# Kernel tuning notes

Measured on AMD Instinct MI355X. Metric: run time of the kernel, lower is better.

The kernel has to match this reference:

```python
import jax, jax.numpy as jnp
import numpy as np

B, N, D = 8, 512, 3


def setup_inputs() -> dict:
    key = jax.random.key(0)
    ks = jax.random.split(key, 9)
    s = lambda fan_in: 1.0 / np.sqrt(fan_in)
    return {
        "coords": jax.random.normal(ks[0], (B, N, D), jnp.float32),
        "fw0": jax.random.normal(ks[1], (3, 64), jnp.float32) * s(3),
        "fb0": jnp.zeros((64,), jnp.float32),
        "fw1": jax.random.normal(ks[2], (64, 128), jnp.float32) * s(64),
        "fb1": jnp.zeros((128,), jnp.float32),
        "aw0": jax.random.normal(ks[3], (6, 64), jnp.float32) * s(6),
        "ab0": jnp.zeros((64,), jnp.float32),
        "aw1": jax.random.normal(ks[4], (64, 64), jnp.float32) * s(64),
        "ab1": jnp.zeros((64,), jnp.float32),
        "aw2": jax.random.normal(ks[5], (64, 1), jnp.float32) * s(64),
        "ab2": jnp.zeros((1,), jnp.float32),
        "uw0": jax.random.normal(ks[6], (259, 256), jnp.float32) * s(259),
        "ub0": jnp.zeros((256,), jnp.float32),
        "uw1": jax.random.normal(ks[7], (256, 128), jnp.float32) * s(256),
        "ub1": jnp.zeros((128,), jnp.float32),
    }


def reference(coords, fw0, fb0, fw1, fb1, aw0, ab0, aw1, ab1, aw2, ab2,
              uw0, ub0, uw1, ub1):
    relu = jax.nn.relu
    # node feature MLP: (B, N, 3) -> (B, N, 128)
    h = relu(relu(coords @ fw0 + fb0) @ fw1 + fb1)
    # pairwise concat: (B, N, N, 2D)
    nP = coords.shape[1]
    pi = jnp.broadcast_to(coords[:, :, None, :], (B, nP, nP, D))
    pj = jnp.broadcast_to(coords[:, None, :, :], (B, nP, nP, D))
    pair = jnp.concatenate([pi, pj], axis=-1)
    # adjacency MLP -> scalar per pair; note final layer also has relu
    a = relu(pair @ aw0 + ab0)
    a = relu(a @ aw1 + ab1)
    A = relu(a @ aw2 + ab2)[..., 0]  # (B, N, N)
    # aggregate
    V = jnp.matmul(A, h)  # (B, N, 128)
    updates = jnp.concatenate([h, coords, V], axis=-1)  # (B, N, 259)
    h_next = relu(relu(updates @ uw0 + ub0) @ uw1 + ub1)
    # max pool over points
    return jnp.max(h_next, axis=1)  # (B, 128)
```

## Files before the change

### kernel.cpp

```cpp
#include <hip/hip_runtime.h>
#include <hip/hip_bf16.h>

#define B_ 8
#define N_ 512

typedef __attribute__((ext_vector_type(8))) __bf16 bf16x8;
typedef __attribute__((ext_vector_type(8))) _Float16 f16x8;
typedef __attribute__((ext_vector_type(2))) _Float16 h2;
typedef __attribute__((ext_vector_type(4))) float f32x4;
typedef __attribute__((ext_vector_type(4))) unsigned int u32x4;

__device__ __forceinline__ unsigned pk_bf16(float hi, float lo) {
    return __builtin_amdgcn_perm(__builtin_bit_cast(unsigned, hi),
                                 __builtin_bit_cast(unsigned, lo), 0x07060302u);
}

__device__ __forceinline__ h2 h2pack(float a, float b) {
    h2 r; r[0] = (_Float16)a; r[1] = (_Float16)b; return r;
}
__device__ __forceinline__ h2 h2splat(float a) {
    _Float16 x = (_Float16)a; h2 r; r[0] = x; r[1] = x; return r;
}

__global__ __launch_bounds__(256) void k_mega(
    const float* __restrict__ coords,
    const float* __restrict__ fw0, const float* __restrict__ fb0,
    const float* __restrict__ fw1, const float* __restrict__ fb1,
    const float* __restrict__ aw0, const float* __restrict__ ab0,
    const float* __restrict__ aw1, const float* __restrict__ ab1,
    const float* __restrict__ aw2, const float* __restrict__ ab2,
    const float* __restrict__ uw0, const float* __restrict__ uw1,
    __bf16* __restrict__ h_bf, __bf16* __restrict__ h_t,
    __bf16* __restrict__ w0t, __bf16* __restrict__ w1t,
    __bf16* __restrict__ A,
    float* __restrict__ out, int out_size)
{
    const int blk = blockIdx.x;
    const int t = threadIdx.x;

    if (blk < 2048) {
        __shared__ __align__(16) _Float16 s_aw1p[4096];
        __shared__ float s_eb[64], s_ew[64];

        {
            const int base = t * 16;
            _Float16 bt[16];
#pragma unroll
            for (int e = 0; e < 16; ++e) {
                int id = base + e;
                int j = id & 7, mm = (id >> 3) & 15, qq = (id >> 7) & 3;
                int ct = (id >> 9) & 3, s = (id >> 11) & 1;
                bt[e] = (_Float16)aw1[(s * 32 + qq * 8 + j) * 64 + ct * 16 + mm];
            }
            *(f16x8*)&s_aw1p[base] = *(f16x8*)&bt[0];
            *(f16x8*)&s_aw1p[base + 8] = *(f16x8*)&bt[8];
            if (t < 64) {
                int qq = t >> 4, ct = (t >> 2) & 3, r = t & 3;
                int ch = ct * 16 + qq * 4 + r;
                s_eb[t] = ab1[ch];
                s_ew[t] = aw2[ch];
            }
        }
        __syncthreads();

        const int l = t & 63;
        const int wave = t >> 6;
        const int q = l >> 4;
        const int m = l & 15;
        const int b = blk >> 8;
        const int half = blk & 1;
        const int i = (((blk >> 1) & 127) << 2) + wave;

        const float* ci = coords + (size_t)(b * N_ + i) * 3;
        const float ci0 = ci[0], ci1 = ci[1], ci2 = ci[2];

        h2 oh[8], w3h[8], w4h[8], w5h[8];
        {
#pragma unroll
            for (int s = 0; s < 2; ++s) {
                int base = s * 32 + q * 8;
                f32x4 bb0 = *(const f32x4*)(ab0 + base);
                f32x4 bb1 = *(const f32x4*)(ab0 + base + 4);
                f32x4 wa0 = *(const f32x4*)(aw0 + base);
                f32x4 wa1 = *(const f32x4*)(aw0 + base + 4);
                f32x4 wb0 = *(const f32x4*)(aw0 + 64 + base);
                f32x4 wb1 = *(const f32x4*)(aw0 + 64 + base + 4);
                f32x4 wc0 = *(const f32x4*)(aw0 + 128 + base);
                f32x4 wc1 = *(const f32x4*)(aw0 + 128 + base + 4);
                f32x4 oa = bb0 + ci0 * wa0 + ci1 * wb0 + ci2 * wc0;
                f32x4 ob = bb1 + ci0 * wa1 + ci1 * wb1 + ci2 * wc1;
                f32x4 w3a = *(const f32x4*)(aw0 + 192 + base);
                f32x4 w3b = *(const f32x4*)(aw0 + 192 + base + 4);
                f32x4 w4a = *(const f32x4*)(aw0 + 256 + base);
                f32x4 w4b = *(const f32x4*)(aw0 + 256 + base + 4);
                f32x4 w5a = *(const f32x4*)(aw0 + 320 + base);
                f32x4 w5b = *(const f32x4*)(aw0 + 320 + base + 4);
                oh[s * 4 + 0] = h2pack(oa[0], oa[1]);
                oh[s * 4 + 1] = h2pack(oa[2], oa[3]);
                oh[s * 4 + 2] = h2pack(ob[0], ob[1]);
                oh[s * 4 + 3] = h2pack(ob[2], ob[3]);
                w3h[s * 4 + 0] = h2pack(w3a[0], w3a[1]);
                w3h[s * 4 + 1] = h2pack(w3a[2], w3a[3]);
                w3h[s * 4 + 2] = h2pack(w3b[0], w3b[1]);
                w3h[s * 4 + 3] = h2pack(w3b[2], w3b[3]);
                w4h[s * 4 + 0] = h2pack(w4a[0], w4a[1]);
                w4h[s * 4 + 1] = h2pack(w4a[2], w4a[3]);
                w4h[s * 4 + 2] = h2pack(w4b[0], w4b[1]);
                w4h[s * 4 + 3] = h2pack(w4b[2], w4b[3]);
                w5h[s * 4 + 0] = h2pack(w5a[0], w5a[1]);
                w5h[s * 4 + 1] = h2pack(w5a[2], w5a[3]);
                w5h[s * 4 + 2] = h2pack(w5b[0], w5b[1]);
                w5h[s * 4 + 3] = h2pack(w5b[2], w5b[3]);
            }
        }

        f16x8 bfr[2][4];
#pragma unroll
        for (int s = 0; s < 2; ++s)
#pragma unroll
            for (int ct = 0; ct < 4; ++ct)
                bfr[s][ct] = *(const f16x8*)&s_aw1p[s * 2048 + ct * 512 + q * 128 + m * 8];

        f32x4 ab1q[4], ewq[4];
#pragma unroll
        for (int ct = 0; ct < 4; ++ct) {
            ab1q[ct] = *(const f32x4*)&s_eb[q * 16 + ct * 4];
            ewq[ct] = *(const f32x4*)&s_ew[q * 16 + ct * 4];
        }
        const float ab2s = ab2[0];

        __bf16* Arow = A + ((size_t)(b * N_ + i) << 9) + half * 256;
        const float* cjbase = coords + (size_t)(b * N_ + half * 256 + m) * 3;
        const h2 zero2 = h2splat(0.0f);

#pragma unroll 1
        for (int tt = 0; tt < 16; ++tt) {
            const float* cj = cjbase + tt * 48;
            h2 d0h = h2splat(cj[0]);
            h2 d1h = h2splat(cj[1]);
            h2 d2h = h2splat(cj[2]);

            u32x4 pa, pb;
#pragma unroll
            for (int k = 0; k < 4; ++k) {
                h2 va = __builtin_elementwise_max(
                    __builtin_elementwise_fma(d0h, w3h[k],
                    __builtin_elementwise_fma(d1h, w4h[k],
                    __builtin_elementwise_fma(d2h, w5h[k], oh[k]))), zero2);
                h2 vb = __builtin_elementwise_max(
                    __builtin_elementwise_fma(d0h, w3h[4 + k],
                    __builtin_elementwise_fma(d1h, w4h[4 + k],
                    __builtin_elementwise_fma(d2h, w5h[4 + k], oh[4 + k]))), zero2);
                pa[k] = __builtin_bit_cast(unsigned, va);
                pb[k] = __builtin_bit_cast(unsigned, vb);
            }
            f16x8 a0 = __builtin_bit_cast(f16x8, pa);
            f16x8 a1 = __builtin_bit_cast(f16x8, pb);

            float p0, p1, p2, p3;
            {
                f32x4 c0v = ab1q[0];
                c0v = __builtin_amdgcn_mfma_f32_16x16x32_f16(bfr[0][0], a0, c0v, 0, 0, 0);
                c0v = __builtin_amdgcn_mfma_f32_16x16x32_f16(bfr[1][0], a1, c0v, 0, 0, 0);
                f32x4 c1v = ab1q[1];
                c1v = __builtin_amdgcn_mfma_f32_16x16x32_f16(bfr[0][1], a0, c1v, 0, 0, 0);
                c1v = __builtin_amdgcn_mfma_f32_16x16x32_f16(bfr[1][1], a1, c1v, 0, 0, 0);
                f32x4 c2v = ab1q[2];
                c2v = __builtin_amdgcn_mfma_f32_16x16x32_f16(bfr[0][2], a0, c2v, 0, 0, 0);
                c2v = __builtin_amdgcn_mfma_f32_16x16x32_f16(bfr[1][2], a1, c2v, 0, 0, 0);
                f32x4 c3v = ab1q[3];
                c3v = __builtin_amdgcn_mfma_f32_16x16x32_f16(bfr[0][3], a0, c3v, 0, 0, 0);
                c3v = __builtin_amdgcn_mfma_f32_16x16x32_f16(bfr[1][3], a1, c3v, 0, 0, 0);
                p0 = fmaxf(c0v[0], 0.f) * ewq[0][0] + fmaxf(c0v[1], 0.f) * ewq[0][1]
                   + fmaxf(c0v[2], 0.f) * ewq[0][2] + fmaxf(c0v[3], 0.f) * ewq[0][3];
                p1 = fmaxf(c1v[0], 0.f) * ewq[1][0] + fmaxf(c1v[1], 0.f) * ewq[1][1]
                   + fmaxf(c1v[2], 0.f) * ewq[1][2] + fmaxf(c1v[3], 0.f) * ewq[1][3];
                p2 = fmaxf(c2v[0], 0.f) * ewq[2][0] + fmaxf(c2v[1], 0.f) * ewq[2][1]
                   + fmaxf(c2v[2], 0.f) * ewq[2][2] + fmaxf(c2v[3], 0.f) * ewq[2][3];
                p3 = fmaxf(c3v[0], 0.f) * ewq[3][0] + fmaxf(c3v[1], 0.f) * ewq[3][1]
                   + fmaxf(c3v[2], 0.f) * ewq[3][2] + fmaxf(c3v[3], 0.f) * ewq[3][3];
            }
            float p = (p0 + p1) + (p2 + p3);
            p += __shfl_xor(p, 16, 64);
            p += __shfl_xor(p, 32, 64);
            if (l < 16) Arow[(tt << 4) + l] = (__bf16)fmaxf(ab2s + p, 0.0f);
        }
    } else if (blk < 3072) {
        const int row0 = (blk - 2048) << 2;
        const int b = row0 >> 9;
        const int n0 = row0 & 511;
        __shared__ float cds4[4][4];
        __shared__ float hid4[4][64];
        if (t < 12) {
            int r = t / 3, d = t - 3 * r;
            cds4[r][d] = coords[(size_t)row0 * 3 + t];
        }
        __syncthreads();
        {
            int r = t >> 6, ch = t & 63;
            float v = fb0[ch];
            v += cds4[r][0] * fw0[0 * 64 + ch];
            v += cds4[r][1] * fw0[1 * 64 + ch];
            v += cds4[r][2] * fw0[2 * 64 + ch];
            hid4[r][ch] = fmaxf(v, 0.0f);
        }
        __syncthreads();
        {
            int ch = t & 127;
            int rp = (t >> 7) << 1;
            float hv0 = fb1[ch], hv1 = hv0;
#pragma unroll 4
            for (int k = 0; k < 64; ++k) {
                float w = fw1[k * 128 + ch];
                hv0 += hid4[rp][k] * w;
                hv1 += hid4[rp + 1][k] * w;
            }
            hv0 = fmaxf(hv0, 0.0f);
            hv1 = fmaxf(hv1, 0.0f);
            h_bf[((size_t)(row0 + rp) << 7) + ch] = (__bf16)hv0;
            h_bf[((size_t)(row0 + rp + 1) << 7) + ch] = (__bf16)hv1;
            *(unsigned*)(h_t + (size_t)(b * 128 + ch) * 512 + n0 + rp) =
                pk_bf16(hv1, hv0);
        }
    } else if (blk < 3328) {
        int k = blk - 3072;
        int c = t;
        int src = (k < 128) ? k : (k + 3);
        w0t[(size_t)c * 256 + k] = (__bf16)uw0[(size_t)src * 256 + c];
    } else if (blk < 3456) {
        int id = (blk - 3328) * 256 + t;
        int c = id & 127, k = id >> 7;
        w1t[(size_t)c * 256 + k] = (__bf16)uw1[(size_t)k * 128 + c];
    } else {
        int i = (blk - 3456) * 256 + t;
        if (i < out_size) out[i] = 0.0f;
    }
}

__global__ __launch_bounds__(1024) void k_aggupd(
    const __bf16* __restrict__ A, const __bf16* __restrict__ h_t,
    const __bf16* __restrict__ h_bf, const float* __restrict__ coords,
    const float* __restrict__ uw0, const float* __restrict__ ub0,
    const __bf16* __restrict__ w0t, const __bf16* __restrict__ w1t,
    const float* __restrict__ ub1,
    float* __restrict__ out)
{
    const int t = threadIdx.x;
    const int w = t >> 6;
    const int gw = w & 7;
    const int ks = w >> 3;
    const int l = t & 63;
    const int q = l >> 4;
    const int m = l & 15;
    const int row0 = blockIdx.x << 4;
    const int b = row0 >> 9;

    __shared__ __align__(16) __bf16 act[16][264];
    __shared__ __align__(16) __bf16 u1[16][264];
    __shared__ float vp[2][16][128];
    __shared__ float cds[16][4];

    {
        unsigned hv = *(const unsigned*)(h_bf + ((size_t)row0 << 7) + t * 2);
        *(unsigned*)&act[(t * 2) >> 7][(t * 2) & 127] = hv;
    }
    if (t < 48) {
        int r = t / 3, d = t - 3 * r;
        cds[r][d] = coords[(size_t)row0 * 3 + t];
    }

    const __bf16* Ar = A + (size_t)(row0 + m) * 512 + ks * 256 + q * 8;
    const __bf16* hp = h_t + ((size_t)b << 16) + (size_t)(gw * 16 + m) * 512
                       + ks * 256 + q * 8;
    f32x4 acc = {0.f, 0.f, 0.f, 0.f};
#pragma unroll 4
    for (int kt = 0; kt < 8; ++kt) {
        bf16x8 av = *(const bf16x8*)(Ar + kt * 32);
        bf16x8 bv = *(const bf16x8*)(hp + kt * 32);
        acc = __builtin_amdgcn_mfma_f32_16x16x32_bf16(av, bv, acc, 0, 0, 0);
    }
#pragma unroll
    for (int r = 0; r < 4; ++r)
        vp[ks][q * 4 + r][gw * 16 + m] = acc[r];
    __syncthreads();

#pragma unroll
    for (int it = 0; it < 2; ++it) {
        int idx = t + it * 1024;
        int row = idx >> 7, ch = idx & 127;
        act[row][128 + ch] = (__bf16)(vp[0][row][ch] + vp[1][row][ch]);
    }
    __syncthreads();

    bf16x8 af[8];
#pragma unroll
    for (int ch = 0; ch < 8; ++ch)
        af[ch] = *(const bf16x8*)&act[m][q * 8 + 32 * ch];
    {
        const int c = w * 16 + m;
        const float wx = uw0[128 * 256 + c];
        const float wy = uw0[129 * 256 + c];
        const float wz = uw0[130 * 256 + c];
        const float bias = ub0[c];
        f32x4 a1c;
#pragma unroll
        for (int r = 0; r < 4; ++r)
            a1c[r] = bias + cds[q * 4 + r][0] * wx + cds[q * 4 + r][1] * wy
                          + cds[q * 4 + r][2] * wz;
        const __bf16* wp = w0t + (size_t)c * 256 + q * 8;
#pragma unroll
        for (int ch = 0; ch < 8; ++ch) {
            bf16x8 bfr = *(const bf16x8*)(wp + 32 * ch);
            a1c = __builtin_amdgcn_mfma_f32_16x16x32_bf16(af[ch], bfr, a1c, 0, 0, 0);
        }
#pragma unroll
        for (int r = 0; r < 4; ++r)
            u1[q * 4 + r][c] = (__bf16)fmaxf(a1c[r], 0.0f);
    }
    __syncthreads();

    if (w < 8) {
        bf16x8 af2[8];
#pragma unroll
        for (int ch = 0; ch < 8; ++ch)
            af2[ch] = *(const bf16x8*)&u1[m][q * 8 + 32 * ch];
        const int c = w * 16 + m;
        float bias = ub1[c];
        f32x4 a2c = {bias, bias, bias, bias};
        const __bf16* wp = w1t + (size_t)c * 256 + q * 8;
#pragma unroll
        for (int ch = 0; ch < 8; ++ch) {
            bf16x8 bfr = *(const bf16x8*)(wp + 32 * ch);
            a2c = __builtin_amdgcn_mfma_f32_16x16x32_bf16(af2[ch], bfr, a2c, 0, 0, 0);
        }
        float mx = fmaxf(fmaxf(a2c[0], a2c[1]), fmaxf(a2c[2], a2c[3]));
        mx = fmaxf(mx, 0.0f);
        mx = fmaxf(mx, __shfl_xor(mx, 16, 64));
        mx = fmaxf(mx, __shfl_xor(mx, 32, 64));
        if (l < 16)
            atomicMax((int*)(out + ((size_t)b << 7) + c), __float_as_int(mx));
    }
}

extern "C" void kernel_launch(void* const* d_in, const int* in_sizes, int n_in,
                              void* d_out, int out_size, void* d_ws, size_t ws_size,
                              hipStream_t stream)
{
    const float* coords = (const float*)d_in[0];
    const float* fw0 = (const float*)d_in[1];
    const float* fb0 = (const float*)d_in[2];
    const float* fw1 = (const float*)d_in[3];
    const float* fb1 = (const float*)d_in[4];
    const float* aw0 = (const float*)d_in[5];
    const float* ab0 = (const float*)d_in[6];
    const float* aw1 = (const float*)d_in[7];
    const float* ab1 = (const float*)d_in[8];
    const float* aw2 = (const float*)d_in[9];
    const float* ab2 = (const float*)d_in[10];
    const float* uw0 = (const float*)d_in[11];
    const float* ub0 = (const float*)d_in[12];
    const float* uw1 = (const float*)d_in[13];
    const float* ub1 = (const float*)d_in[14];
    float* out = (float*)d_out;

    char* ws = (char*)d_ws;
    __bf16* A    = (__bf16*)(ws);
    __bf16* h_t  = (__bf16*)(ws + (4u << 20));
    __bf16* h_bf = (__bf16*)(ws + (5u << 20));
    __bf16* w0t  = (__bf16*)(ws + (6u << 20));
    __bf16* w1t  = (__bf16*)(ws + (6u << 20) + (128u << 10));

    k_mega<<<3460, 256, 0, stream>>>(coords, fw0, fb0, fw1, fb1,
                                     aw0, ab0, aw1, ab1, aw2, ab2, uw0, uw1,
                                     h_bf, h_t, w0t, w1t, A, out, out_size);
    k_aggupd<<<256, 1024, 0, stream>>>(A, h_t, h_bf, coords, uw0, ub0,
                                       w0t, w1t, ub1, out);
}
```

Measured before the change: 142.0 us.

## Move pairwise layer-0 and final projection of adjacency MLP onto MFMA

The first adjacency layer, previously computed with packed-half FMAs per lane, now runs as four 16x16x16 f16 MFMAs. The per-pair coordinates are augmented with a constant 1 so the precomputed i-dependent bias folds into the product. Pair coordinates are staged once per block in LDS as packed halves. The final 64-to-1 projection is also done with MFMAs, replacing scalar multiply-adds and cross-lane shuffles, and fp32-to-half conversions use cvt_pkrtz. This offloads VALU work to the matrix cores, at the cost of extra MFMA issue slots, mostly-zero operand lanes and round-toward-zero fp16 precision.

```diff
diff --git a/kernel.cpp b/kernel.cpp
--- a/kernel.cpp
+++ b/kernel.cpp
@@ -6,20 +6,26 @@
 
 typedef __attribute__((ext_vector_type(8))) __bf16 bf16x8;
 typedef __attribute__((ext_vector_type(8))) _Float16 f16x8;
+typedef __attribute__((ext_vector_type(4))) _Float16 f16x4;
 typedef __attribute__((ext_vector_type(2))) _Float16 h2;
 typedef __attribute__((ext_vector_type(4))) float f32x4;
 typedef __attribute__((ext_vector_type(4))) unsigned int u32x4;
+typedef __attribute__((ext_vector_type(2))) unsigned int u32x2;
 
 __device__ __forceinline__ unsigned pk_bf16(float hi, float lo) {
     return __builtin_amdgcn_perm(__builtin_bit_cast(unsigned, hi),
                                  __builtin_bit_cast(unsigned, lo), 0x07060302u);
 }
 
-__device__ __forceinline__ h2 h2pack(float a, float b) {
-    h2 r; r[0] = (_Float16)a; r[1] = (_Float16)b; return r;
-}
-__device__ __forceinline__ h2 h2splat(float a) {
-    _Float16 x = (_Float16)a; h2 r; r[0] = x; r[1] = x; return r;
+__device__ __forceinline__ h2 pkrtz(float a, float b) {
+    return __builtin_bit_cast(h2, __builtin_amdgcn_cvt_pkrtz(a, b));
+}
+__device__ __forceinline__ unsigned pkrtz_u(float a, float b) {
+    return __builtin_bit_cast(unsigned, __builtin_amdgcn_cvt_pkrtz(a, b));
+}
+__device__ __forceinline__ unsigned relu2_u(h2 v) {
+    const h2 z2 = {(_Float16)0.0f, (_Float16)0.0f};
+    return __builtin_bit_cast(unsigned, __builtin_elementwise_max(v, z2));
 }
 
 __global__ __launch_bounds__(256) void k_mega(
@@ -40,7 +46,11 @@
 
     if (blk < 2048) {
         __shared__ __align__(16) _Float16 s_aw1p[4096];
-        __shared__ float s_eb[64], s_ew[64];
+        __shared__ float s_eb[64];
+        __shared__ __align__(8) unsigned s_cj[256][2];
+
+        const int b = blk >> 8;
+        const int half = blk & 1;
 
         {
             const int base = t * 16;
@@ -56,10 +66,11 @@
             *(f16x8*)&s_aw1p[base + 8] = *(f16x8*)&bt[8];
             if (t < 64) {
                 int qq = t >> 4, ct = (t >> 2) & 3, r = t & 3;
-                int ch = ct * 16 + qq * 4 + r;
-                s_eb[t] = ab1[ch];
-                s_ew[t] = aw2[ch];
+                s_eb[t] = ab1[ct * 16 + qq * 4 + r];
             }
+            const float* cj = coords + (size_t)(b * N_ + half * 256 + t) * 3;
+            s_cj[t][0] = pkrtz_u(cj[0], cj[1]);
+            s_cj[t][1] = pkrtz_u(cj[2], 1.0f);
         }
         __syncthreads();
 
@@ -67,51 +78,36 @@
         const int wave = t >> 6;
         const int q = l >> 4;
         const int m = l & 15;
-        const int b = blk >> 8;
-        const int half = blk & 1;
         const int i = (((blk >> 1) & 127) << 2) + wave;
 
         const float* ci = coords + (size_t)(b * N_ + i) * 3;
         const float ci0 = ci[0], ci1 = ci[1], ci2 = ci[2];
 
-        h2 oh[8], w3h[8], w4h[8], w5h[8];
+        f16x4 a0f[4];
         {
-#pragma unroll
-            for (int s = 0; s < 2; ++s) {
-                int base = s * 32 + q * 8;
-                f32x4 bb0 = *(const f32x4*)(ab0 + base);
-                f32x4 bb1 = *(const f32x4*)(ab0 + base + 4);
-                f32x4 wa0 = *(const f32x4*)(aw0 + base);
-                f32x4 wa1 = *(const f32x4*)(aw0 + base + 4);
-                f32x4 wb0 = *(const f32x4*)(aw0 + 64 + base);
-                f32x4 wb1 = *(const f32x4*)(aw0 + 64 + base + 4);
-                f32x4 wc0 = *(const f32x4*)(aw0 + 128 + base);
-                f32x4 wc1 = *(const f32x4*)(aw0 + 128 + base + 4);
-                f32x4 oa = bb0 + ci0 * wa0 + ci1 * wb0 + ci2 * wc0;
-                f32x4 ob = bb1 + ci0 * wa1 + ci1 * wb1 + ci2 * wc1;
-                f32x4 w3a = *(const f32x4*)(aw0 + 192 + base);
-                f32x4 w3b = *(const f32x4*)(aw0 + 192 + base + 4);
-                f32x4 w4a = *(const f32x4*)(aw0 + 256 + base);
-                f32x4 w4b = *(const f32x4*)(aw0 + 256 + base + 4);
-                f32x4 w5a = *(const f32x4*)(aw0 + 320 + base);
-                f32x4 w5b = *(const f32x4*)(aw0 + 320 + base + 4);
-                oh[s * 4 + 0] = h2pack(oa[0], oa[1]);
-                oh[s * 4 + 1] = h2pack(oa[2], oa[3]);
-                oh[s * 4 + 2] = h2pack(ob[0], ob[1]);
-                oh[s * 4 + 3] = h2pack(ob[2], ob[3]);
-                w3h[s * 4 + 0] = h2pack(w3a[0], w3a[1]);
-                w3h[s * 4 + 1] = h2pack(w3a[2], w3a[3]);
-                w3h[s * 4 + 2] = h2pack(w3b[0], w3b[1]);
-                w3h[s * 4 + 3] = h2pack(w3b[2], w3b[3]);
-                w4h[s * 4 + 0] = h2pack(w4a[0], w4a[1]);
-                w4h[s * 4 + 1] = h2pack(w4a[2], w4a[3]);
-                w4h[s * 4 + 2] = h2pack(w4b[0], w4b[1]);
-                w4h[s * 4 + 3] = h2pack(w4b[2], w4b[3]);
-                w5h[s * 4 + 0] = h2pack(w5a[0], w5a[1]);
-                w5h[s * 4 + 1] = h2pack(w5a[2], w5a[3]);
-                w5h[s * 4 + 2] = h2pack(w5b[0], w5b[1]);
-                w5h[s * 4 + 3] = h2pack(w5b[2], w5b[3]);
+            const int chb = ((m >> 2) << 3) + (m & 3);
+            const int offs[4] = {0, 4, 32, 36};
+#pragma unroll
+            for (int t4 = 0; t4 < 4; ++t4) {
+                const int ch = chb + offs[t4];
+                float w3 = aw0[192 + ch], w4 = aw0[256 + ch], w5 = aw0[320 + ch];
+                float o = ab0[ch] + ci0 * aw0[ch] + ci1 * aw0[64 + ch]
+                                  + ci2 * aw0[128 + ch];
+                u32x2 fr;
+                fr[0] = (q == 0) ? pkrtz_u(w3, w4) : 0u;
+                fr[1] = (q == 0) ? pkrtz_u(w5, o) : 0u;
+                a0f[t4] = __builtin_bit_cast(f16x4, fr);
             }
+        }
+
+        f16x4 ewf[4];
+#pragma unroll
+        for (int ct = 0; ct < 4; ++ct) {
+            const float* ep = aw2 + ct * 16 + (q << 2);
+            u32x2 fr;
+            fr[0] = pkrtz_u(ep[0], ep[1]);
+            fr[1] = pkrtz_u(ep[2], ep[3]);
+            ewf[ct] = __builtin_bit_cast(f16x4, fr);
         }
 
         f16x8 bfr[2][4];
@@ -121,69 +117,67 @@
             for (int ct = 0; ct < 4; ++ct)
                 bfr[s][ct] = *(const f16x8*)&s_aw1p[s * 2048 + ct * 512 + q * 128 + m * 8];
 
-        f32x4 ab1q[4], ewq[4];
-#pragma unroll
-        for (int ct = 0; ct < 4; ++ct) {
+        f32x4 ab1q[4];
+#pragma unroll
+        for (int ct = 0; ct < 4; ++ct)
             ab1q[ct] = *(const f32x4*)&s_eb[q * 16 + ct * 4];
-            ewq[ct] = *(const f32x4*)&s_ew[q * 16 + ct * 4];
-        }
+
         const float ab2s = ab2[0];
+        const f32x4 pr0 = {ab2s, ab2s, ab2s, ab2s};
+        const f32x4 zf = {0.f, 0.f, 0.f, 0.f};
 
         __bf16* Arow = A + ((size_t)(b * N_ + i) << 9) + half * 256;
-        const float* cjbase = coords + (size_t)(b * N_ + half * 256 + m) * 3;
-        const h2 zero2 = h2splat(0.0f);
 
 #pragma unroll 1
         for (int tt = 0; tt < 16; ++tt) {
-            const float* cj = cjbase + tt * 48;
-            h2 d0h = h2splat(cj[0]);
-            h2 d1h = h2splat(cj[1]);
-            h2 d2h = h2splat(cj[2]);
+            f16x4 bj = __builtin_bit_cast(f16x4, *(const u32x2*)s_cj[(tt << 4) + m]);
+
+            f32x4 d0 = __builtin_amdgcn_mfma_f32_16x16x16f16(a0f[0], bj, zf, 0, 0, 0);
+            f32x4 d1 = __builtin_amdgcn_mfma_f32_16x16x16f16(a0f[1], bj, zf, 0, 0, 0);
+            f32x4 d2 = __builtin_amdgcn_mfma_f32_16x16x16f16(a0f[2], bj, zf, 0, 0, 0);
+            f32x4 d3 = __builtin_amdgcn_mfma_f32_16x16x16f16(a0f[3], bj, zf, 0, 0, 0);
 
             u32x4 pa, pb;
-#pragma unroll
-            for (int k = 0; k < 4; ++k) {
-                h2 va = __builtin_elementwise_max(
-                    __builtin_elementwise_fma(d0h, w3h[k],
-                    __builtin_elementwise_fma(d1h, w4h[k],
-                    __builtin_elementwise_fma(d2h, w5h[k], oh[k]))), zero2);
-                h2 vb = __builtin_elementwise_max(
-                    __builtin_elementwise_fma(d0h, w3h[4 + k],
-                    __builtin_elementwise_fma(d1h, w4h[4 + k],
-                    __builtin_elementwise_fma(d2h, w5h[4 + k], oh[4 + k]))), zero2);
-                pa[k] = __builtin_bit_cast(unsigned, va);
-                pb[k] = __builtin_bit_cast(unsigned, vb);
-            }
+            pa[0] = relu2_u(pkrtz(d0[0], d0[1]));
+            pa[1] = relu2_u(pkrtz(d0[2], d0[3]));
+            pa[2] = relu2_u(pkrtz(d1[0], d1[1]));
+            pa[3] = relu2_u(pkrtz(d1[2], d1[3]));
+            pb[0] = relu2_u(pkrtz(d2[0], d2[1]));
+            pb[1] = relu2_u(pkrtz(d2[2], d2[3]));
+            pb[2] = relu2_u(pkrtz(d3[0], d3[1]));
+            pb[3] = relu2_u(pkrtz(d3[2], d3[3]));
             f16x8 a0 = __builtin_bit_cast(f16x8, pa);
             f16x8 a1 = __builtin_bit_cast(f16x8, pb);
 
-            float p0, p1, p2, p3;
-            {
-                f32x4 c0v = ab1q[0];
-                c0v = __builtin_amdgcn_mfma_f32_16x16x32_f16(bfr[0][0], a0, c0v, 0, 0, 0);
-                c0v = __builtin_amdgcn_mfma_f32_16x16x32_f16(bfr[1][0], a1, c0v, 0, 0, 0);
-                f32x4 c1v = ab1q[1];
-                c1v = __builtin_amdgcn_mfma_f32_16x16x32_f16(bfr[0][1], a0, c1v, 0, 0, 0);
-                c1v = __builtin_amdgcn_mfma_f32_16x16x32_f16(bfr[1][1], a1, c1v, 0, 0, 0);
-                f32x4 c2v = ab1q[2];
-                c2v = __builtin_amdgcn_mfma_f32_16x16x32_f16(bfr[0][2], a0, c2v, 0, 0, 0);
-                c2v = __builtin_amdgcn_mfma_f32_16x16x32_f16(bfr[1][2], a1, c2v, 0, 0, 0);
-                f32x4 c3v = ab1q[3];
-                c3v = __builtin_amdgcn_mfma_f32_16x16x32_f16(bfr[0][3], a0, c3v, 0, 0, 0);
-                c3v = __builtin_amdgcn_mfma_f32_16x16x32_f16(bfr[1][3], a1, c3v, 0, 0, 0);
-                p0 = fmaxf(c0v[0], 0.f) * ewq[0][0] + fmaxf(c0v[1], 0.f) * ewq[0][1]
-                   + fmaxf(c0v[2], 0.f) * ewq[0][2] + fmaxf(c0v[3], 0.f) * ewq[0][3];
-                p1 = fmaxf(c1v[0], 0.f) * ewq[1][0] + fmaxf(c1v[1], 0.f) * ewq[1][1]
-                   + fmaxf(c1v[2], 0.f) * ewq[1][2] + fmaxf(c1v[3], 0.f) * ewq[1][3];
-                p2 = fmaxf(c2v[0], 0.f) * ewq[2][0] + fmaxf(c2v[1], 0.f) * ewq[2][1]
-                   + fmaxf(c2v[2], 0.f) * ewq[2][2] + fmaxf(c2v[3], 0.f) * ewq[2][3];
-                p3 = fmaxf(c3v[0], 0.f) * ewq[3][0] + fmaxf(c3v[1], 0.f) * ewq[3][1]
-                   + fmaxf(c3v[2], 0.f) * ewq[3][2] + fmaxf(c3v[3], 0.f) * ewq[3][3];
-            }
-            float p = (p0 + p1) + (p2 + p3);
-            p += __shfl_xor(p, 16, 64);
-            p += __shfl_xor(p, 32, 64);
-            if (l < 16) Arow[(tt << 4) + l] = (__bf16)fmaxf(ab2s + p, 0.0f);
+            f32x4 c0v = __builtin_amdgcn_mfma_f32_16x16x32_f16(bfr[0][0], a0, ab1q[0], 0, 0, 0);
+            c0v = __builtin_amdgcn_mfma_f32_16x16x32_f16(bfr[1][0], a1, c0v, 0, 0, 0);
+            f32x4 c1v = __builtin_amdgcn_mfma_f32_16x16x32_f16(bfr[0][1], a0, ab1q[1], 0, 0, 0);
+            c1v = __builtin_amdgcn_mfma_f32_16x16x32_f16(bfr[1][1], a1, c1v, 0, 0, 0);
+            f32x4 c2v = __builtin_amdgcn_mfma_f32_16x16x32_f16(bfr[0][2], a0, ab1q[2], 0, 0, 0);
+            c2v = __builtin_amdgcn_mfma_f32_16x16x32_f16(bfr[1][2], a1, c2v, 0, 0, 0);
+            f32x4 c3v = __builtin_amdgcn_mfma_f32_16x16x32_f16(bfr[0][3], a0, ab1q[3], 0, 0, 0);
+            c3v = __builtin_amdgcn_mfma_f32_16x16x32_f16(bfr[1][3], a1, c3v, 0, 0, 0);
+
+            u32x2 r0, r1, r2, r3;
+            r0[0] = relu2_u(pkrtz(c0v[0], c0v[1]));
+            r0[1] = relu2_u(pkrtz(c0v[2], c0v[3]));
+            r1[0] = relu2_u(pkrtz(c1v[0], c1v[1]));
+            r1[1] = relu2_u(pkrtz(c1v[2], c1v[3]));
+            r2[0] = relu2_u(pkrtz(c2v[0], c2v[1]));
+            r2[1] = relu2_u(pkrtz(c2v[2], c2v[3]));
+            r3[0] = relu2_u(pkrtz(c3v[0], c3v[1]));
+            r3[1] = relu2_u(pkrtz(c3v[2], c3v[3]));
+
+            f32x4 pr = __builtin_amdgcn_mfma_f32_16x16x16f16(
+                ewf[0], __builtin_bit_cast(f16x4, r0), pr0, 0, 0, 0);
+            pr = __builtin_amdgcn_mfma_f32_16x16x16f16(
+                ewf[1], __builtin_bit_cast(f16x4, r1), pr, 0, 0, 0);
+            pr = __builtin_amdgcn_mfma_f32_16x16x16f16(
+                ewf[2], __builtin_bit_cast(f16x4, r2), pr, 0, 0, 0);
+            pr = __builtin_amdgcn_mfma_f32_16x16x16f16(
+                ewf[3], __builtin_bit_cast(f16x4, r3), pr, 0, 0, 0);
+
+            if (l < 16) Arow[(tt << 4) + l] = (__bf16)fmaxf(pr[0], 0.0f);
         }
     } else if (blk < 3072) {
         const int row0 = (blk - 2048) << 2;
```

Result: faster. 128.2 us (-9.8%).
